# Kernel optimization log

Measured on AMD Instinct MI355X. Metric: run time of the kernel, lower is better.

Reference implementation:

```python
import jax, jax.numpy as jnp
import numpy as np

N = 50000      # nodes
E = 800000     # edges (avg degree 16)
IN = 256       # in_features
F1 = 32        # gnn_features per head
F2 = 32        # out_features per head
H = 8          # heads
NEG_SLOPE = 0.2


def setup_inputs() -> dict:
    key = jax.random.key(0)
    ks = jax.random.split(key, 12)
    s = 0.05
    return {
        "x":   jax.random.normal(ks[0], (N, IN), jnp.float32),
        "W1":  jax.random.normal(ks[1], (IN, H * F1), jnp.float32) * s,
        "al1": jax.random.normal(ks[2], (H, F1), jnp.float32) * s,
        "ar1": jax.random.normal(ks[3], (H, F1), jnp.float32) * s,
        "b1":  jnp.zeros((H, F1), jnp.float32),
        "W2":  jax.random.normal(ks[4], (F1, H * F2), jnp.float32) * s,
        "al2": jax.random.normal(ks[5], (H, F2), jnp.float32) * s,
        "ar2": jax.random.normal(ks[6], (H, F2), jnp.float32) * s,
        "b2":  jnp.zeros((H, F2), jnp.float32),
        "src": jax.random.randint(ks[7], (E,), 0, N, jnp.int32),
        "dst": jax.random.randint(ks[8], (E,), 0, N, jnp.int32),
    }


def _gat_layer(x, W, al, ar, b, src, dst):
    """One DGL-style GATConv. x:[N,Fin] -> [N,H,F]."""
    n, h, f = x.shape[0], al.shape[0], al.shape[1]
    z = (x @ W).reshape(n, h, f)                      # [N,H,F] projected feats
    el = jnp.einsum('nhf,hf->nh', z, al)              # src attention logits
    er = jnp.einsum('nhf,hf->nh', z, ar)              # dst attention logits
    e = el[src] + er[dst]                             # [E,H]
    e = jnp.where(e >= 0, e, NEG_SLOPE * e)           # LeakyReLU(0.2)
    # segmented (per-destination) softmax over incoming edges
    m = jax.ops.segment_max(e, dst, num_segments=n)   # [N,H]
    ex = jnp.exp(e - m[dst])                          # [E,H]
    denom = jax.ops.segment_sum(ex, dst, num_segments=n)
    alpha = ex / denom[dst]                           # [E,H]
    # weighted scatter-aggregate
    out = jax.ops.segment_sum(alpha[:, :, None] * z[src], dst, num_segments=n)
    return out + b[None]                              # [N,H,F]


def reference(x, W1, al1, ar1, b1, W2, al2, ar2, b2, src, dst):
    h = _gat_layer(x, W1, al1, ar1, b1, src, dst).mean(axis=1)   # [N,F1]
    h = jax.nn.elu(h)                                            # Dropout(0.5) = identity in eval
    out = _gat_layer(h, W2, al2, ar2, b2, src, dst).mean(axis=1) # [N,F2]
    return out
```

## Files before the change

kernel.cpp:

```cpp
#include <hip/hip_runtime.h>
#include <hip/hip_fp16.h>
#include <math.h>

#define IN_F 256
#define NHEAD 8
#define FDIM 32
#define SCAN_B 512

typedef _Float16 f16x8 __attribute__((ext_vector_type(8)));
typedef float f32x4 __attribute__((ext_vector_type(4)));

__device__ inline unsigned pkh2(float x, float y) {
  __half2 h = __floats2half2_rn(x, y);
  return *reinterpret_cast<unsigned*>(&h);
}


__global__ __launch_bounds__(256) void hist_k(const int* __restrict__ dst,
                                              int* __restrict__ deg, int E) {
  int i = blockIdx.x * 256 + threadIdx.x;
  if (i < E) atomicAdd(&deg[dst[i]], 1);
}

__global__ __launch_bounds__(SCAN_B) void scan1_k(const int* __restrict__ deg,
                                                  int* __restrict__ offs,
                                                  int* __restrict__ bsum, int N) {
  __shared__ int s[SCAN_B];
  int t = threadIdx.x;
  int i = blockIdx.x * SCAN_B + t;
  s[t] = (i < N) ? deg[i] : 0;
  __syncthreads();
  for (int off = 1; off < SCAN_B; off <<= 1) {
    int add = (t >= off) ? s[t - off] : 0;
    __syncthreads();
    s[t] += add;
    __syncthreads();
  }
  if (i < N) offs[i + 1] = s[t];
  if (t == SCAN_B - 1) bsum[blockIdx.x] = s[t];
}

__global__ __launch_bounds__(SCAN_B) void scan2_k(int* __restrict__ bsum, int nb) {
  __shared__ int s[SCAN_B];
  int t = threadIdx.x;
  s[t] = (t < nb) ? bsum[t] : 0;
  __syncthreads();
  for (int off = 1; off < SCAN_B; off <<= 1) {
    int add = (t >= off) ? s[t - off] : 0;
    __syncthreads();
    s[t] += add;
    __syncthreads();
  }
  if (t < nb) bsum[t] = (t == 0) ? 0 : s[t - 1];
}

__global__ __launch_bounds__(SCAN_B) void scan3_k(int* __restrict__ offs,
                                                  const int* __restrict__ bsum, int N) {
  int i = blockIdx.x * SCAN_B + threadIdx.x;
  if (i < N) offs[i + 1] += bsum[blockIdx.x];
  if (i == 0) offs[0] = 0;
}

__global__ __launch_bounds__(256) void scatter_k(const int* __restrict__ src,
                                                 const int* __restrict__ dst,
                                                 const int* __restrict__ offs,
                                                 int* __restrict__ cursor,
                                                 int* __restrict__ esrc, int E) {
  int i = blockIdx.x * 256 + threadIdx.x;
  if (i < E) {
    int d = dst[i];
    int pos = offs[d] + atomicAdd(&cursor[d], 1);
    esrc[pos] = src[i];
  }
}

__global__ __launch_bounds__(256) void w1cvt_k(const float* __restrict__ W1,
                                               __half* __restrict__ W1t) {
  __shared__ float s[16][17];
  int bx = blockIdx.x * 16, by = blockIdx.y * 16;
  int tx = threadIdx.x, ty = threadIdx.y;
  s[ty][tx] = W1[(by + ty) * 256 + bx + tx];
  __syncthreads();
  W1t[(size_t)(bx + ty) * 256 + by + tx] = __float2half(s[tx][ty]);
}

__global__ __launch_bounds__(512, 1) void gemm_xw_mfma_k(const float* __restrict__ X,
                                                         const __half* __restrict__ W1t,
                                                         __half* __restrict__ Zh, int M) {
  __shared__ __half Ws[256 * 256];
  int t = threadIdx.x;

#pragma unroll
  for (int i = 0; i < 16; ++i) {
    int chunk = t + i * 512;
    int col = chunk >> 5;
    int g = chunk & 31;
    f16x8 v = *reinterpret_cast<const f16x8*>(W1t + (size_t)col * 256 + g * 8);
    int gs = g ^ (col & 31);
    *reinterpret_cast<f16x8*>(&Ws[col * 256 + gs * 8]) = v;
  }

  int wid = t >> 6, l = t & 63;
  int r = l & 15, kg = l >> 4;
  int row0 = blockIdx.x * 256 + wid * 32;

  int rowA0 = row0 + r;
  int rowA1 = row0 + 16 + r;
  int rc0 = (rowA0 < M) ? rowA0 : (M - 1);
  int rc1 = (rowA1 < M) ? rowA1 : (M - 1);
  const float* xp0 = X + (size_t)rc0 * 256 + kg * 8;
  const float* xp1 = X + (size_t)rc1 * 256 + kg * 8;
  f16x8 a0[8], a1[8];
#pragma unroll
  for (int ks = 0; ks < 8; ++ks) {
    float4 f0 = *reinterpret_cast<const float4*>(xp0 + ks * 32);
    float4 f1 = *reinterpret_cast<const float4*>(xp0 + ks * 32 + 4);
    f16x8 av;
    av[0] = (_Float16)f0.x; av[1] = (_Float16)f0.y;
    av[2] = (_Float16)f0.z; av[3] = (_Float16)f0.w;
    av[4] = (_Float16)f1.x; av[5] = (_Float16)f1.y;
    av[6] = (_Float16)f1.z; av[7] = (_Float16)f1.w;
    a0[ks] = av;
    float4 g0 = *reinterpret_cast<const float4*>(xp1 + ks * 32);
    float4 g1 = *reinterpret_cast<const float4*>(xp1 + ks * 32 + 4);
    f16x8 bv;
    bv[0] = (_Float16)g0.x; bv[1] = (_Float16)g0.y;
    bv[2] = (_Float16)g0.z; bv[3] = (_Float16)g0.w;
    bv[4] = (_Float16)g1.x; bv[5] = (_Float16)g1.y;
    bv[6] = (_Float16)g1.z; bv[7] = (_Float16)g1.w;
    a1[ks] = bv;
  }

  __syncthreads();

  int orow0 = row0 + kg * 4;
  int orow1 = row0 + 16 + kg * 4;

#pragma unroll
  for (int nf = 0; nf < 16; ++nf) {
    int colb = nf * 16 + r;
    int cbase = colb * 256;
    int cx = colb & 31;
    f16x8 b0 = *reinterpret_cast<const f16x8*>(&Ws[cbase + ((0 * 4 + kg) ^ cx) * 8]);
    f16x8 b1 = *reinterpret_cast<const f16x8*>(&Ws[cbase + ((1 * 4 + kg) ^ cx) * 8]);
    f16x8 b2 = *reinterpret_cast<const f16x8*>(&Ws[cbase + ((2 * 4 + kg) ^ cx) * 8]);
    f16x8 b3 = *reinterpret_cast<const f16x8*>(&Ws[cbase + ((3 * 4 + kg) ^ cx) * 8]);
    f16x8 b4 = *reinterpret_cast<const f16x8*>(&Ws[cbase + ((4 * 4 + kg) ^ cx) * 8]);
    f16x8 b5 = *reinterpret_cast<const f16x8*>(&Ws[cbase + ((5 * 4 + kg) ^ cx) * 8]);
    f16x8 b6 = *reinterpret_cast<const f16x8*>(&Ws[cbase + ((6 * 4 + kg) ^ cx) * 8]);
    f16x8 b7 = *reinterpret_cast<const f16x8*>(&Ws[cbase + ((7 * 4 + kg) ^ cx) * 8]);

    f32x4 e0 = {0.f, 0.f, 0.f, 0.f}, e1 = {0.f, 0.f, 0.f, 0.f};
    f32x4 f0 = {0.f, 0.f, 0.f, 0.f}, f1 = {0.f, 0.f, 0.f, 0.f};
    e0 = __builtin_amdgcn_mfma_f32_16x16x32_f16(a0[0], b0, e0, 0, 0, 0);
    e1 = __builtin_amdgcn_mfma_f32_16x16x32_f16(a0[1], b1, e1, 0, 0, 0);
    f0 = __builtin_amdgcn_mfma_f32_16x16x32_f16(a1[0], b0, f0, 0, 0, 0);
    f1 = __builtin_amdgcn_mfma_f32_16x16x32_f16(a1[1], b1, f1, 0, 0, 0);
    e0 = __builtin_amdgcn_mfma_f32_16x16x32_f16(a0[2], b2, e0, 0, 0, 0);
    e1 = __builtin_amdgcn_mfma_f32_16x16x32_f16(a0[3], b3, e1, 0, 0, 0);
    f0 = __builtin_amdgcn_mfma_f32_16x16x32_f16(a1[2], b2, f0, 0, 0, 0);
    f1 = __builtin_amdgcn_mfma_f32_16x16x32_f16(a1[3], b3, f1, 0, 0, 0);
    e0 = __builtin_amdgcn_mfma_f32_16x16x32_f16(a0[4], b4, e0, 0, 0, 0);
    e1 = __builtin_amdgcn_mfma_f32_16x16x32_f16(a0[5], b5, e1, 0, 0, 0);
    f0 = __builtin_amdgcn_mfma_f32_16x16x32_f16(a1[4], b4, f0, 0, 0, 0);
    f1 = __builtin_amdgcn_mfma_f32_16x16x32_f16(a1[5], b5, f1, 0, 0, 0);
    e0 = __builtin_amdgcn_mfma_f32_16x16x32_f16(a0[6], b6, e0, 0, 0, 0);
    e1 = __builtin_amdgcn_mfma_f32_16x16x32_f16(a0[7], b7, e1, 0, 0, 0);
    f0 = __builtin_amdgcn_mfma_f32_16x16x32_f16(a1[6], b6, f0, 0, 0, 0);
    f1 = __builtin_amdgcn_mfma_f32_16x16x32_f16(a1[7], b7, f1, 0, 0, 0);
    f32x4 s0 = e0 + e1;
    f32x4 s1 = f0 + f1;
#pragma unroll
    for (int i = 0; i < 4; ++i) {
      if (orow0 + i < M)
        Zh[(size_t)(orow0 + i) * 256 + nf * 16 + r] = __float2half((float)s0[i]);
    }
#pragma unroll
    for (int i = 0; i < 4; ++i) {
      if (orow1 + i < M)
        Zh[(size_t)(orow1 + i) * 256 + nf * 16 + r] = __float2half((float)s1[i]);
    }
  }
}

__global__ __launch_bounds__(256) void gemm_h_k(const float* __restrict__ Hmat,
                                                const float* __restrict__ W2,
                                                __half* __restrict__ Zh, int M) {
  __shared__ float Ws[32][256];
  __shared__ float Hs[32][20];
  int t = threadIdx.x;
  for (int i = t; i < 32 * 256; i += 256) Ws[i >> 8][i & 255] = W2[i];
  int row0 = blockIdx.x * 16;
  for (int i = t; i < 16 * 32; i += 256) {
    int r = i >> 5, k = i & 31;
    Hs[k][r] = (row0 + r < M) ? Hmat[(size_t)(row0 + r) * 32 + k] : 0.f;
  }
  __syncthreads();
  int tx = t & 63, ty = t >> 6;
  float acc[4][4] = {};
#pragma unroll
  for (int k = 0; k < 32; ++k) {
    float4 a4 = *reinterpret_cast<const float4*>(&Hs[k][ty * 4]);
    float4 b4 = *reinterpret_cast<const float4*>(&Ws[k][tx * 4]);
    float a[4] = {a4.x, a4.y, a4.z, a4.w};
    float b[4] = {b4.x, b4.y, b4.z, b4.w};
#pragma unroll
    for (int i = 0; i < 4; ++i)
#pragma unroll
      for (int j = 0; j < 4; ++j) acc[i][j] = fmaf(a[i], b[j], acc[i][j]);
  }
#pragma unroll
  for (int i = 0; i < 4; ++i) {
    int r = row0 + ty * 4 + i;
    if (r < M) {
      uint2 w;
      w.x = pkh2(acc[i][0], acc[i][1]);
      w.y = pkh2(acc[i][2], acc[i][3]);
      *reinterpret_cast<uint2*>(&Zh[(size_t)r * 256 + tx * 4]) = w;
    }
  }
}

__global__ __launch_bounds__(256) void logits_k(const __half* __restrict__ Zh,
                                                const float* __restrict__ al,
                                                const float* __restrict__ ar,
                                                float* __restrict__ el,
                                                float* __restrict__ er, int N) {
  int wave = threadIdx.x >> 6;
  int lane = threadIdx.x & 63;
  int n = blockIdx.x * 4 + wave;
  if (n >= N) return;
  uint2 u = *reinterpret_cast<const uint2*>(&Zh[(size_t)n * 256 + lane * 4]);
  float2 f0 = __half22float2(*reinterpret_cast<__half2*>(&u.x));
  float2 f1 = __half22float2(*reinterpret_cast<__half2*>(&u.y));
  float4 a4 = reinterpret_cast<const float4*>(al)[lane];
  float4 r4 = reinterpret_cast<const float4*>(ar)[lane];
  float pl = f0.x * a4.x + f0.y * a4.y + f1.x * a4.z + f1.y * a4.w;
  float pr = f0.x * r4.x + f0.y * r4.y + f1.x * r4.z + f1.y * r4.w;
  pl += __shfl_xor(pl, 1); pl += __shfl_xor(pl, 2); pl += __shfl_xor(pl, 4);
  pr += __shfl_xor(pr, 1); pr += __shfl_xor(pr, 2); pr += __shfl_xor(pr, 4);
  if ((lane & 7) == 0) {
    int h = lane >> 3;
    el[(size_t)n * 8 + h] = pl;
    er[(size_t)n * 8 + h] = pr;
  }
}

__global__ __launch_bounds__(256) void alpha_k(const float* __restrict__ el,
                                               const float* __restrict__ er,
                                               const int* __restrict__ offs,
                                               const int* __restrict__ esrc,
                                               float* __restrict__ alf,
                                               float* __restrict__ rden, int N) {
  int g = blockIdx.x * 256 + threadIdx.x;
  if (g >= N * NHEAD) return;
  int n = g >> 3, h = g & 7;
  int beg = offs[n], end = offs[n + 1];
  float er_h = er[g];
  float m = -INFINITY;
  for (int i = beg; i < end; ++i) {
    float e = el[(size_t)esrc[i] * 8 + h] + er_h;
    e = (e >= 0.f) ? e : 0.2f * e;
    m = fmaxf(m, e);
  }
  float s = 0.f;
  for (int i = beg; i < end; ++i) {
    float e = el[(size_t)esrc[i] * 8 + h] + er_h;
    e = (e >= 0.f) ? e : 0.2f * e;
    float ex = __expf(e - m);
    alf[(size_t)i * 8 + h] = ex;
    s += ex;
  }
  rden[g] = (end > beg) ? 1.f / s : 0.f;
}

template <bool LAYER1>
__global__ __launch_bounds__(256) void agg_k(const __half* __restrict__ Zh,
                                             const float* __restrict__ alf,
                                             const float* __restrict__ rden,
                                             const float* __restrict__ bias,
                                             const int* __restrict__ offs,
                                             const int* __restrict__ esrc,
                                             float* __restrict__ out, int N) {
  int wid = threadIdx.x >> 6, lane = threadIdx.x & 63;
  int n = blockIdx.x * 4 + wid;
  if (n >= N) return;
  int h = lane >> 3, q = lane & 7;
  int beg = offs[n], end = offs[n + 1];
  float4 acc = make_float4(0.f, 0.f, 0.f, 0.f);
#pragma unroll 4
  for (int i = beg; i < end; ++i) {
    int sidx = esrc[i];
    float a = alf[(size_t)i * 8 + h];
    uint2 u = *reinterpret_cast<const uint2*>(&Zh[(size_t)sidx * 256 + h * 32 + q * 4]);
    float2 f0 = __half22float2(*reinterpret_cast<__half2*>(&u.x));
    float2 f1 = __half22float2(*reinterpret_cast<__half2*>(&u.y));
    acc.x = fmaf(a, f0.x, acc.x);
    acc.y = fmaf(a, f0.y, acc.y);
    acc.z = fmaf(a, f1.x, acc.z);
    acc.w = fmaf(a, f1.y, acc.w);
  }
  float r = rden[(size_t)n * 8 + h];
  float4 b4 = *reinterpret_cast<const float4*>(&bias[h * 32 + q * 4]);
  float4 v;
  v.x = fmaf(acc.x, r, b4.x);
  v.y = fmaf(acc.y, r, b4.y);
  v.z = fmaf(acc.z, r, b4.z);
  v.w = fmaf(acc.w, r, b4.w);
#pragma unroll
  for (int off = 8; off < 64; off <<= 1) {
    v.x += __shfl_xor(v.x, off);
    v.y += __shfl_xor(v.y, off);
    v.z += __shfl_xor(v.z, off);
    v.w += __shfl_xor(v.w, off);
  }
  if (h == 0) {
    v.x *= 0.125f; v.y *= 0.125f; v.z *= 0.125f; v.w *= 0.125f;
    if (LAYER1) {
      v.x = (v.x > 0.f) ? v.x : expm1f(v.x);
      v.y = (v.y > 0.f) ? v.y : expm1f(v.y);
      v.z = (v.z > 0.f) ? v.z : expm1f(v.z);
      v.w = (v.w > 0.f) ? v.w : expm1f(v.w);
    }
    *reinterpret_cast<float4*>(&out[(size_t)n * 32 + q * 4]) = v;
  }
}


extern "C" void kernel_launch(void* const* d_in, const int* in_sizes, int n_in,
                              void* d_out, int out_size, void* d_ws, size_t ws_size,
                              hipStream_t stream) {
  const float* x   = (const float*)d_in[0];
  const float* W1  = (const float*)d_in[1];
  const float* al1 = (const float*)d_in[2];
  const float* ar1 = (const float*)d_in[3];
  const float* b1  = (const float*)d_in[4];
  const float* W2  = (const float*)d_in[5];
  const float* al2 = (const float*)d_in[6];
  const float* ar2 = (const float*)d_in[7];
  const float* b2  = (const float*)d_in[8];
  const int* src   = (const int*)d_in[9];
  const int* dst   = (const int*)d_in[10];
  float* out = (float*)d_out;

  const int N = in_sizes[0] / IN_F;
  const int E = in_sizes[9];

  char* p = (char*)d_ws;
  auto alloc = [&](size_t bytes) {
    char* q = p;
    p += (bytes + 255) & ~(size_t)255;
    return q;
  };
  __half* zh  = (__half*)alloc((size_t)N * 256 * 2);
  __half* w1t = (__half*)alloc((size_t)256 * 256 * 2);
  float* el   = (float*)alloc((size_t)N * 8 * 4);
  float* er   = (float*)alloc((size_t)N * 8 * 4);
  float* h1   = (float*)alloc((size_t)N * 32 * 4);
  float* alf  = (float*)alloc((size_t)E * 8 * 4);
  float* rden = (float*)alloc((size_t)N * 8 * 4);
  int* offs   = (int*)alloc((size_t)(N + 1) * 4);
  int* deg    = (int*)alloc((size_t)N * 4);
  int* cursor = (int*)alloc((size_t)N * 4);
  int* bsum   = (int*)alloc((size_t)SCAN_B * 4);
  int* esrc   = (int*)alloc((size_t)E * 4);

  hipMemsetAsync(deg, 0, (size_t)N * 4, stream);
  hipMemsetAsync(cursor, 0, (size_t)N * 4, stream);

  int nb = (N + SCAN_B - 1) / SCAN_B;
  hist_k<<<(E + 255) / 256, 256, 0, stream>>>(dst, deg, E);
  scan1_k<<<nb, SCAN_B, 0, stream>>>(deg, offs, bsum, N);
  scan2_k<<<1, SCAN_B, 0, stream>>>(bsum, nb);
  scan3_k<<<nb, SCAN_B, 0, stream>>>(offs, bsum, N);
  scatter_k<<<(E + 255) / 256, 256, 0, stream>>>(src, dst, offs, cursor, esrc, E);

  int nh_blocks = (N * NHEAD + 255) / 256;

  w1cvt_k<<<dim3(16, 16), dim3(16, 16), 0, stream>>>(W1, w1t);
  gemm_xw_mfma_k<<<(N + 255) / 256, 512, 0, stream>>>(x, w1t, zh, N);
  logits_k<<<(N + 3) / 4, 256, 0, stream>>>(zh, al1, ar1, el, er, N);
  alpha_k<<<nh_blocks, 256, 0, stream>>>(el, er, offs, esrc, alf, rden, N);
  agg_k<true><<<(N + 3) / 4, 256, 0, stream>>>(zh, alf, rden, b1, offs, esrc, h1, N);

  gemm_h_k<<<(N + 15) / 16, 256, 0, stream>>>(h1, W2, zh, N);
  logits_k<<<(N + 3) / 4, 256, 0, stream>>>(zh, al2, ar2, el, er, N);
  alpha_k<<<nh_blocks, 256, 0, stream>>>(el, er, offs, esrc, alf, rden, N);
  agg_k<false><<<(N + 3) / 4, 256, 0, stream>>>(zh, alf, rden, b2, offs, esrc, out, N);
}
```

Measured before the change: 439.2 us.

## Fuse segmented softmax into aggregation kernel, dropping per-edge alpha buffer

Replaces the separate alpha_k and agg_k kernels with one wave-per-node kernel. It computes the per-destination max cooperatively across lanes, then recomputes the exponentials in chunks of 64 edges, staging them in LDS before the weighted gather over Z. This removes the E×8 float alpha buffer's write and read-back and one launch per layer. In exchange the el gather is repeated and there is extra LDS traffic and wave barriers per chunk.

```diff
diff --git a/kernel.cpp b/kernel.cpp
--- a/kernel.cpp
+++ b/kernel.cpp
@@ -246,62 +246,65 @@
   }
 }
 
-__global__ __launch_bounds__(256) void alpha_k(const float* __restrict__ el,
-                                               const float* __restrict__ er,
-                                               const int* __restrict__ offs,
-                                               const int* __restrict__ esrc,
-                                               float* __restrict__ alf,
-                                               float* __restrict__ rden, int N) {
-  int g = blockIdx.x * 256 + threadIdx.x;
-  if (g >= N * NHEAD) return;
-  int n = g >> 3, h = g & 7;
+template <bool LAYER1>
+__global__ __launch_bounds__(256) void aggf_k(const __half* __restrict__ Zh,
+                                              const float* __restrict__ el,
+                                              const float* __restrict__ er,
+                                              const float* __restrict__ bias,
+                                              const int* __restrict__ offs,
+                                              const int* __restrict__ esrc,
+                                              float* __restrict__ out, int N) {
+  __shared__ float plds[4][64][8];
+  int wid = threadIdx.x >> 6, lane = threadIdx.x & 63;
+  int n = blockIdx.x * 4 + wid;
+  if (n >= N) return;
+  int h = lane >> 3;
+  int sub = lane & 7;
   int beg = offs[n], end = offs[n + 1];
-  float er_h = er[g];
-  float m = -INFINITY;
-  for (int i = beg; i < end; ++i) {
+  float er_h = er[(size_t)n * 8 + h];
+
+  float m = -1e30f;
+  for (int i = beg + sub; i < end; i += 8) {
     float e = el[(size_t)esrc[i] * 8 + h] + er_h;
     e = (e >= 0.f) ? e : 0.2f * e;
     m = fmaxf(m, e);
   }
+  m = fmaxf(m, __shfl_xor(m, 1));
+  m = fmaxf(m, __shfl_xor(m, 2));
+  m = fmaxf(m, __shfl_xor(m, 4));
+
   float s = 0.f;
-  for (int i = beg; i < end; ++i) {
-    float e = el[(size_t)esrc[i] * 8 + h] + er_h;
-    e = (e >= 0.f) ? e : 0.2f * e;
-    float ex = __expf(e - m);
-    alf[(size_t)i * 8 + h] = ex;
-    s += ex;
-  }
-  rden[g] = (end > beg) ? 1.f / s : 0.f;
-}
-
-template <bool LAYER1>
-__global__ __launch_bounds__(256) void agg_k(const __half* __restrict__ Zh,
-                                             const float* __restrict__ alf,
-                                             const float* __restrict__ rden,
-                                             const float* __restrict__ bias,
-                                             const int* __restrict__ offs,
-                                             const int* __restrict__ esrc,
-                                             float* __restrict__ out, int N) {
-  int wid = threadIdx.x >> 6, lane = threadIdx.x & 63;
-  int n = blockIdx.x * 4 + wid;
-  if (n >= N) return;
-  int h = lane >> 3, q = lane & 7;
-  int beg = offs[n], end = offs[n + 1];
   float4 acc = make_float4(0.f, 0.f, 0.f, 0.f);
-#pragma unroll 4
-  for (int i = beg; i < end; ++i) {
-    int sidx = esrc[i];
-    float a = alf[(size_t)i * 8 + h];
-    uint2 u = *reinterpret_cast<const uint2*>(&Zh[(size_t)sidx * 256 + h * 32 + q * 4]);
-    float2 f0 = __half22float2(*reinterpret_cast<__half2*>(&u.x));
-    float2 f1 = __half22float2(*reinterpret_cast<__half2*>(&u.y));
-    acc.x = fmaf(a, f0.x, acc.x);
-    acc.y = fmaf(a, f0.y, acc.y);
-    acc.z = fmaf(a, f1.x, acc.z);
-    acc.w = fmaf(a, f1.y, acc.w);
-  }
-  float r = rden[(size_t)n * 8 + h];
-  float4 b4 = *reinterpret_cast<const float4*>(&bias[h * 32 + q * 4]);
+  for (int cbeg = beg; cbeg < end; cbeg += 64) {
+    int cnt = min(64, end - cbeg);
+    for (int j = sub; j < cnt; j += 8) {
+      float e = el[(size_t)esrc[cbeg + j] * 8 + h] + er_h;
+      e = (e >= 0.f) ? e : 0.2f * e;
+      float p = __expf(e - m);
+      s += p;
+      plds[wid][j][h] = p;
+    }
+    asm volatile("s_waitcnt lgkmcnt(0)" ::: "memory");
+    __builtin_amdgcn_wave_barrier();
+    for (int j = 0; j < cnt; ++j) {
+      int sidx = esrc[cbeg + j];
+      float p = plds[wid][j][h];
+      uint2 u = *reinterpret_cast<const uint2*>(&Zh[(size_t)sidx * 256 + h * 32 + sub * 4]);
+      float2 f0 = __half22float2(*reinterpret_cast<__half2*>(&u.x));
+      float2 f1 = __half22float2(*reinterpret_cast<__half2*>(&u.y));
+      acc.x = fmaf(p, f0.x, acc.x);
+      acc.y = fmaf(p, f0.y, acc.y);
+      acc.z = fmaf(p, f1.x, acc.z);
+      acc.w = fmaf(p, f1.y, acc.w);
+    }
+    __builtin_amdgcn_wave_barrier();
+  }
+
+  s += __shfl_xor(s, 1);
+  s += __shfl_xor(s, 2);
+  s += __shfl_xor(s, 4);
+  float r = (end > beg) ? 1.f / s : 0.f;
+  float4 b4 = *reinterpret_cast<const float4*>(&bias[h * 32 + sub * 4]);
   float4 v;
   v.x = fmaf(acc.x, r, b4.x);
   v.y = fmaf(acc.y, r, b4.y);
@@ -322,7 +325,7 @@
       v.z = (v.z > 0.f) ? v.z : expm1f(v.z);
       v.w = (v.w > 0.f) ? v.w : expm1f(v.w);
     }
-    *reinterpret_cast<float4*>(&out[(size_t)n * 32 + q * 4]) = v;
+    *reinterpret_cast<float4*>(&out[(size_t)n * 32 + sub * 4]) = v;
   }
 }
 
@@ -357,8 +360,6 @@
   float* el   = (float*)alloc((size_t)N * 8 * 4);
   float* er   = (float*)alloc((size_t)N * 8 * 4);
   float* h1   = (float*)alloc((size_t)N * 32 * 4);
-  float* alf  = (float*)alloc((size_t)E * 8 * 4);
-  float* rden = (float*)alloc((size_t)N * 8 * 4);
   int* offs   = (int*)alloc((size_t)(N + 1) * 4);
   int* deg    = (int*)alloc((size_t)N * 4);
   int* cursor = (int*)alloc((size_t)N * 4);
@@ -375,16 +376,12 @@
   scan3_k<<<nb, SCAN_B, 0, stream>>>(offs, bsum, N);
   scatter_k<<<(E + 255) / 256, 256, 0, stream>>>(src, dst, offs, cursor, esrc, E);
 
-  int nh_blocks = (N * NHEAD + 255) / 256;
-
   w1cvt_k<<<dim3(16, 16), dim3(16, 16), 0, stream>>>(W1, w1t);
   gemm_xw_mfma_k<<<(N + 255) / 256, 512, 0, stream>>>(x, w1t, zh, N);
   logits_k<<<(N + 3) / 4, 256, 0, stream>>>(zh, al1, ar1, el, er, N);
-  alpha_k<<<nh_blocks, 256, 0, stream>>>(el, er, offs, esrc, alf, rden, N);
-  agg_k<true><<<(N + 3) / 4, 256, 0, stream>>>(zh, alf, rden, b1, offs, esrc, h1, N);
+  aggf_k<true><<<(N + 3) / 4, 256, 0, stream>>>(zh, el, er, b1, offs, esrc, h1, N);
 
   gemm_h_k<<<(N + 15) / 16, 256, 0, stream>>>(h1, W2, zh, N);
   logits_k<<<(N + 3) / 4, 256, 0, stream>>>(zh, al2, ar2, el, er, N);
-  alpha_k<<<nh_blocks, 256, 0, stream>>>(el, er, offs, esrc, alf, rden, N);
-  agg_k<false><<<(N + 3) / 4, 256, 0, stream>>>(zh, alf, rden, b2, offs, esrc, out, N);
-}
+  aggf_k<false><<<(N + 3) / 4, 256, 0, stream>>>(zh, el, er, b2, offs, esrc, out, N);
+}
```

Measured after the change: 421.5 us. 1.04x faster.
